# Kernel optimization log

Hardware: AMD Instinct MI355X
Metric: run time of the kernel (lower is better)

The kernel has to match this reference:

```python
import jax, jax.numpy as jnp
import numpy as np

B, S, D = 2, 2048, 1024
H, HD = 16, 64  # num_heads, head_dim; D == H*HD


def setup_inputs() -> dict:
    key = jax.random.key(0)
    k_x, k_wa, k_wp = jax.random.split(key, 3)
    x = jax.random.normal(k_x, (B, S, D), dtype=jnp.float32)
    w_attn = jax.random.normal(k_wa, (D, 3 * D), dtype=jnp.float32) * (1.0 / np.sqrt(D))
    b_attn = jnp.zeros((3 * D,), dtype=jnp.float32)
    w_proj = jax.random.normal(k_wp, (D, D), dtype=jnp.float32) * (1.0 / np.sqrt(D))
    b_proj = jnp.zeros((D,), dtype=jnp.float32)
    return {"x": x, "w_attn": w_attn, "b_attn": b_attn, "w_proj": w_proj, "b_proj": b_proj}


def reference(x, w_attn, b_attn, w_proj, b_proj):
    # c_attn: [B,S,D] -> [B,S,3D], split into q,k,v
    qkv = jnp.einsum('bsd,df->bsf', x, w_attn) + b_attn
    q, k, v = jnp.split(qkv, 3, axis=-1)
    # split heads: [B,S,D] -> [B,S,H,HD]
    q = q.reshape(B, S, H, HD)
    k = k.reshape(B, S, H, HD)
    v = v.reshape(B, S, H, HD)
    scale = 1.0 / jnp.sqrt(jnp.float32(HD))
    # scores: [B,H,S,S]
    scores = jnp.einsum('bnhd,bmhd->bhnm', q, k) * scale
    causal_mask = jnp.tril(jnp.ones((S, S), dtype=jnp.bool_))
    scores = jnp.where(causal_mask, scores, jnp.float32(-1e9))
    attn = jax.nn.softmax(scores, axis=-1)
    # dropout is identity (inference=True / p=0)
    out = jnp.einsum('bhnm,bmhd->bnhd', attn, v)
    out = out.reshape(B, S, D)
    out = jnp.einsum('bsd,de->bse', out, w_proj) + b_proj
    return out
```

## Files before the change

### kernel.cpp

```cpp
#include <hip/hip_runtime.h>

#define Bn 2
#define Sn 2048
#define Dn 1024
#define Hn 16
#define HDn 64

typedef unsigned short u16;
typedef u16 u16x4 __attribute__((ext_vector_type(4)));
typedef u16 u16x8 __attribute__((ext_vector_type(8)));
typedef __bf16 bf16x8 __attribute__((ext_vector_type(8)));
typedef float f32x4 __attribute__((ext_vector_type(4)));

__device__ __forceinline__ u16 cvt1(float f) {
  __bf16 h = (__bf16)f;
  return __builtin_bit_cast(u16, h);
}

__device__ __forceinline__ f32x4 mfma16(u16x8 a, u16x8 b, f32x4 c) {
  return __builtin_amdgcn_mfma_f32_16x16x32_bf16(
      __builtin_bit_cast(bf16x8, a), __builtin_bit_cast(bf16x8, b), c, 0, 0, 0);
}

__device__ __forceinline__ int swzb(int row, int bytecol) {
  return row * 128 + (bytecol ^ ((((row & 7) ^ ((row >> 3) & 7))) << 4));
}

__global__ __launch_bounds__(256) void k_cvt(const float* __restrict__ in,
                                             u16* __restrict__ out, int n4) {
  int i = blockIdx.x * 256 + threadIdx.x;
  if (i < n4) {
    const float4 v = reinterpret_cast<const float4*>(in)[i];
    u16x4 o = {cvt1(v.x), cvt1(v.y), cvt1(v.z), cvt1(v.w)};
    reinterpret_cast<u16x4*>(out)[i] = o;
  }
}

__global__ __launch_bounds__(256) void k_transpose(const float* __restrict__ in,
                                                   u16* __restrict__ out,
                                                   int K, int N) {
  __shared__ u16 tile[32][33];
  const int n0 = blockIdx.x * 32, k0 = blockIdx.y * 32;
  const int tx = threadIdx.x, ty = threadIdx.y;
#pragma unroll
  for (int r = 0; r < 4; ++r) {
    const int k = ty * 4 + r;
    tile[k][tx] = cvt1(in[(size_t)(k0 + k) * N + n0 + tx]);
  }
  __syncthreads();
#pragma unroll
  for (int r = 0; r < 4; ++r) {
    const int n = ty * 4 + r;
    out[(size_t)(n0 + n) * K + k0 + tx] = tile[tx][n];
  }
}

__global__ __launch_bounds__(256) void k_gemm_bt(
    const u16* __restrict__ A, const u16* __restrict__ Bt, int K,
    const float* __restrict__ bias, u16* __restrict__ oq, u16* __restrict__ ok,
    u16* __restrict__ ov, float* __restrict__ of, int mode) {
  __shared__ __align__(16) u16 a_lds[2][128 * 32];
  __shared__ __align__(16) u16 b_lds[2][128 * 32];
  const int tid = threadIdx.x;
  const int lane = tid & 63, w = tid >> 6;
  const int wr = w >> 1, wc = w & 1;
  const int lm = lane & 15, lk = lane >> 4;
  const int m0 = blockIdx.y * 128, n0 = blockIdx.x * 128;

  f32x4 acc[4][4] = {};

#define STAGE(d, ko)                                                          \
  {                                                                           \
    _Pragma("unroll") for (int p = 0; p < 2; ++p) {                           \
      const int e = p * 2048 + w * 512 + lane * 8;                            \
      const int row = e >> 5, col = e & 31;                                   \
      __builtin_amdgcn_global_load_lds(                                       \
          (const __attribute__((address_space(1))) void*)(A + (size_t)(m0 + row) * K + (ko) + col), \
          (__attribute__((address_space(3))) void*)(a_lds[d] + p * 2048 + w * 512), \
          16, 0, 0);                                                          \
      __builtin_amdgcn_global_load_lds(                                       \
          (const __attribute__((address_space(1))) void*)(Bt + (size_t)(n0 + row) * K + (ko) + col), \
          (__attribute__((address_space(3))) void*)(b_lds[d] + p * 2048 + w * 512), \
          16, 0, 0);                                                          \
    }                                                                         \
  }

  STAGE(0, 0);
  __syncthreads();
  int cur = 0;
  for (int k0 = 0; k0 < K; k0 += 32) {
    if (k0 + 32 < K) STAGE(cur ^ 1, k0 + 32);
    u16x8 av[4], bv[4];
#pragma unroll
    for (int m = 0; m < 4; ++m)
      av[m] = *reinterpret_cast<const u16x8*>(a_lds[cur] + (wr * 64 + m * 16 + lm) * 32 + lk * 8);
#pragma unroll
    for (int n = 0; n < 4; ++n)
      bv[n] = *reinterpret_cast<const u16x8*>(b_lds[cur] + (wc * 64 + n * 16 + lm) * 32 + lk * 8);
#pragma unroll
    for (int m = 0; m < 4; ++m)
#pragma unroll
      for (int n = 0; n < 4; ++n)
        acc[m][n] = mfma16(av[m], bv[n], acc[m][n]);
    __syncthreads();
    cur ^= 1;
  }
#undef STAGE

#pragma unroll
  for (int m = 0; m < 4; ++m) {
#pragma unroll
    for (int n = 0; n < 4; ++n) {
      const int col = n0 + wc * 64 + n * 16 + lm;
      const float bb = bias[col];
#pragma unroll
      for (int j = 0; j < 4; ++j) {
        const int row = m0 + wr * 64 + m * 16 + lk * 4 + j;
        float val = acc[m][n][j] + bb;
        if (mode == 0) {
          const int which = col >> 10;
          const int h = (col >> 6) & 15, hd = col & 63;
          if (which == 0) val *= 0.125f;
          const int b = row >> 11, s = row & 2047;
          const size_t idx = (((size_t)(b * Hn + h)) * Sn + s) * HDn + hd;
          u16* dst = which == 0 ? oq : (which == 1 ? ok : ov);
          dst[idx] = cvt1(val);
        } else {
          of[(size_t)row * Dn + col] = val;
        }
      }
    }
  }
}

__global__ __launch_bounds__(256) void k_attn(const u16* __restrict__ qb,
                                              const u16* __restrict__ kb,
                                              const u16* __restrict__ vb,
                                              u16* __restrict__ ob) {
  const int bx = blockIdx.x;
  const int qt = 31 - (bx >> 5);
  const int bh = bx & 31;
  const int h = bh & 15, b = bh >> 4;
  const int tid = threadIdx.x, lane = tid & 63, w = tid >> 6;
  const int lm = lane & 15, lk = lane >> 4;
  const int Q0 = qt * 64;
  const int q0 = Q0 + w * 16;
  const size_t head = (size_t)(b * Hn + h) * Sn * HDn;
  const u16* Q = qb + head;
  const u16* Kp = kb + head;
  const u16* Vp = vb + head;

  __shared__ __align__(16) u16 k_lds[64 * 64];
  __shared__ __align__(16) u16 vt_lds[64 * 64];
  __shared__ __align__(16) u16 p_lds[4][16 * 64];
  char* myp = (char*)p_lds[w];

  const int sr = tid >> 2, scb = (tid & 3) * 16;
  const u16* Ksrc = Kp + (size_t)sr * HDn + scb;
  const u16* Vsrc = Vp + (size_t)sr * HDn + scb;

  u16x8 aq[2];
#pragma unroll
  for (int c = 0; c < 2; ++c)
    aq[c] = *reinterpret_cast<const u16x8*>(Q + (size_t)(q0 + lm) * HDn + c * 32 + lk * 8);

  f32x4 o_acc[4] = {};
  float mrow = -1e30f, lrow = 0.f;
  const float C = 1.44269504f;

  const int nk = Q0 + 64;
  u16x8 kreg[2], vreg[2];
  kreg[0] = *reinterpret_cast<const u16x8*>(Ksrc);
  kreg[1] = *reinterpret_cast<const u16x8*>(Ksrc + 8);
  vreg[0] = *reinterpret_cast<const u16x8*>(Vsrc);
  vreg[1] = *reinterpret_cast<const u16x8*>(Vsrc + 8);

  for (int j0 = 0; j0 < nk; j0 += 64) {
    *reinterpret_cast<u16x8*>((char*)k_lds + swzb(sr, scb * 2)) = kreg[0];
    *reinterpret_cast<u16x8*>((char*)k_lds + swzb(sr, scb * 2 + 16)) = kreg[1];
#pragma unroll
    for (int i = 0; i < 8; ++i) {
      *reinterpret_cast<u16*>((char*)vt_lds + swzb(scb + i, sr * 2)) = vreg[0][i];
      *reinterpret_cast<u16*>((char*)vt_lds + swzb(scb + 8 + i, sr * 2)) = vreg[1][i];
    }
    __syncthreads();
    if (j0 + 64 < nk) {
      const u16* kn = Ksrc + (size_t)(j0 + 64) * HDn;
      const u16* vn = Vsrc + (size_t)(j0 + 64) * HDn;
      kreg[0] = *reinterpret_cast<const u16x8*>(kn);
      kreg[1] = *reinterpret_cast<const u16x8*>(kn + 8);
      vreg[0] = *reinterpret_cast<const u16x8*>(vn);
      vreg[1] = *reinterpret_cast<const u16x8*>(vn + 8);
    }

    f32x4 s[4];
    __builtin_amdgcn_s_setprio(1);
#pragma unroll
    for (int kc = 0; kc < 4; ++kc) {
      const u16x8 kf0 = *reinterpret_cast<const u16x8*>((char*)k_lds + swzb(kc * 16 + lm, lk * 16));
      const u16x8 kf1 = *reinterpret_cast<const u16x8*>((char*)k_lds + swzb(kc * 16 + lm, 64 + lk * 16));
      f32x4 z = {};
      z = mfma16(kf0, aq[0], z);
      s[kc] = mfma16(kf1, aq[1], z);
    }
    __builtin_amdgcn_s_setprio(0);
    if (j0 + 63 > q0) {
#pragma unroll
      for (int kc = 0; kc < 4; ++kc)
#pragma unroll
        for (int jj = 0; jj < 4; ++jj)
          if (j0 + kc * 16 + lk * 4 + jj > q0 + lm) s[kc][jj] = -1e30f;
    }

    float vmax = -1e30f;
#pragma unroll
    for (int kc = 0; kc < 4; ++kc)
#pragma unroll
      for (int jj = 0; jj < 4; ++jj) vmax = fmaxf(vmax, s[kc][jj]);
    vmax = fmaxf(vmax, __shfl_xor(vmax, 16, 64));
    vmax = fmaxf(vmax, __shfl_xor(vmax, 32, 64));
    if (!__all(vmax - mrow <= 8.0f)) {
      const float mnew = fmaxf(mrow, vmax);
      const float alpha = exp2f((mrow - mnew) * C);
      mrow = mnew;
      lrow *= alpha;
      float a4[4];
#pragma unroll
      for (int jj = 0; jj < 4; ++jj) a4[jj] = __shfl(alpha, lk * 4 + jj, 64);
#pragma unroll
      for (int t = 0; t < 4; ++t)
#pragma unroll
        for (int jj = 0; jj < 4; ++jj) o_acc[t][jj] *= a4[jj];
    }
    const float mc = mrow * C;
    float psum = 0.f;
#pragma unroll
    for (int kc = 0; kc < 4; ++kc) {
      u16x4 pk;
#pragma unroll
      for (int jj = 0; jj < 4; ++jj) {
        const float p = exp2f(s[kc][jj] * C - mc);
        psum += p;
        pk[jj] = cvt1(p);
      }
      *reinterpret_cast<u16x4*>(myp + swzb(lm, kc * 32 + lk * 8)) = pk;
    }
    psum += __shfl_xor(psum, 16, 64);
    psum += __shfl_xor(psum, 32, 64);
    lrow += psum;

    __builtin_amdgcn_s_setprio(1);
#pragma unroll
    for (int kt = 0; kt < 2; ++kt) {
      const u16x8 pa = *reinterpret_cast<const u16x8*>(myp + swzb(lm, kt * 64 + lk * 16));
#pragma unroll
      for (int t = 0; t < 4; ++t) {
        const u16x8 vf = *reinterpret_cast<const u16x8*>((char*)vt_lds + swzb(t * 16 + lm, kt * 64 + lk * 16));
        o_acc[t] = mfma16(pa, vf, o_acc[t]);
      }
    }
    __builtin_amdgcn_s_setprio(0);
    __syncthreads();
  }

  float l4[4];
#pragma unroll
  for (int jj = 0; jj < 4; ++jj) l4[jj] = __shfl(lrow, lk * 4 + jj, 64);
#pragma unroll
  for (int t = 0; t < 4; ++t) {
#pragma unroll
    for (int jj = 0; jj < 4; ++jj) {
      const int rowg = q0 + lk * 4 + jj;
      const float val = o_acc[t][jj] / l4[jj];
      ob[((size_t)(b * Sn + rowg)) * Dn + h * HDn + t * 16 + lm] = cvt1(val);
    }
  }
}

extern "C" void kernel_launch(void* const* d_in, const int* in_sizes, int n_in,
                              void* d_out, int out_size, void* d_ws, size_t ws_size,
                              hipStream_t stream) {
  const float* x = (const float*)d_in[0];
  const float* w_attn = (const float*)d_in[1];
  const float* b_attn = (const float*)d_in[2];
  const float* w_proj = (const float*)d_in[3];
  const float* b_proj = (const float*)d_in[4];
  float* out = (float*)d_out;

  u16* ws = (u16*)d_ws;
  u16* xb = ws;
  u16* wat = xb + (size_t)4096 * 1024;
  u16* wpt = wat + (size_t)3072 * 1024;
  u16* qb = wpt + (size_t)1024 * 1024;
  u16* kb = qb + (size_t)Bn * Hn * Sn * HDn;
  u16* vb = kb + (size_t)Bn * Hn * Sn * HDn;
  u16* ao = vb + (size_t)Bn * Hn * Sn * HDn;

  k_cvt<<<4096, 256, 0, stream>>>(x, xb, 1048576);
  k_transpose<<<dim3(3072 / 32, 1024 / 32), dim3(32, 8), 0, stream>>>(w_attn, wat, 1024, 3072);
  k_transpose<<<dim3(1024 / 32, 1024 / 32), dim3(32, 8), 0, stream>>>(w_proj, wpt, 1024, 1024);
  k_gemm_bt<<<dim3(3072 / 128, 4096 / 128), 256, 0, stream>>>(xb, wat, 1024, b_attn, qb, kb, vb, nullptr, 0);
  k_attn<<<Bn * Hn * (Sn / 64), 256, 0, stream>>>(qb, kb, vb, ao);
  k_gemm_bt<<<dim3(1024 / 128, 4096 / 128), 256, 0, stream>>>(ao, wpt, 1024, b_proj, nullptr, nullptr, nullptr, out, 1);
}
```

Before: 202.8 us.

## Rework GEMM to 512 threads with K=64 swizzled tiles and emit V transposed

The projection GEMM now runs 8 waves per block with a 64-wide K step, XOR-swizzled LDS staging and raised MFMA priority. This is meant to reduce LDS bank conflicts and per-iteration sync overhead. The QKV epilogue writes V in a transposed [HD][S] layout, so the attention kernel can stage V^T with vector LDS stores instead of scalar transposing stores. The trade-offs are higher LDS use per block and strided 4-element stores for V in the epilogue.

```diff
diff --git a/kernel.cpp b/kernel.cpp
--- a/kernel.cpp
+++ b/kernel.cpp
@@ -22,8 +22,11 @@
       __builtin_bit_cast(bf16x8, a), __builtin_bit_cast(bf16x8, b), c, 0, 0, 0);
 }
 
+__device__ __forceinline__ int xorv(int row) {
+  return (row & 7) ^ ((row >> 3) & 7);
+}
 __device__ __forceinline__ int swzb(int row, int bytecol) {
-  return row * 128 + (bytecol ^ ((((row & 7) ^ ((row >> 3) & 7))) << 4));
+  return row * 128 + (bytecol ^ (xorv(row) << 4));
 }
 
 __global__ __launch_bounds__(256) void k_cvt(const float* __restrict__ in,
@@ -55,79 +58,101 @@
   }
 }
 
-__global__ __launch_bounds__(256) void k_gemm_bt(
+__global__ __launch_bounds__(512) void k_gemm2(
     const u16* __restrict__ A, const u16* __restrict__ Bt, int K,
     const float* __restrict__ bias, u16* __restrict__ oq, u16* __restrict__ ok,
     u16* __restrict__ ov, float* __restrict__ of, int mode) {
-  __shared__ __align__(16) u16 a_lds[2][128 * 32];
-  __shared__ __align__(16) u16 b_lds[2][128 * 32];
+  __shared__ __align__(16) u16 a_lds[2][8192];
+  __shared__ __align__(16) u16 b_lds[2][8192];
   const int tid = threadIdx.x;
   const int lane = tid & 63, w = tid >> 6;
-  const int wr = w >> 1, wc = w & 1;
+  const int wr = w >> 2, wc = w & 3;
   const int lm = lane & 15, lk = lane >> 4;
   const int m0 = blockIdx.y * 128, n0 = blockIdx.x * 128;
-
-  f32x4 acc[4][4] = {};
-
-#define STAGE(d, ko)                                                          \
+  const int NT = K >> 6;
+
+  const int srow0 = tid >> 3;
+  const int scb = (tid & 7) * 16;
+
+  f32x4 acc[4][2] = {};
+
+#define STAGE2(d, kt)                                                         \
   {                                                                           \
     _Pragma("unroll") for (int p = 0; p < 2; ++p) {                           \
-      const int e = p * 2048 + w * 512 + lane * 8;                            \
-      const int row = e >> 5, col = e & 31;                                   \
+      const int row = p * 64 + srow0;                                         \
+      const int col = (scb ^ (xorv(row) << 4)) >> 1;                          \
       __builtin_amdgcn_global_load_lds(                                       \
-          (const __attribute__((address_space(1))) void*)(A + (size_t)(m0 + row) * K + (ko) + col), \
-          (__attribute__((address_space(3))) void*)(a_lds[d] + p * 2048 + w * 512), \
+          (const __attribute__((address_space(1))) void*)(A + (size_t)(m0 + row) * K + (kt) * 64 + col), \
+          (__attribute__((address_space(3))) void*)(a_lds[d] + p * 4096 + tid * 8), \
           16, 0, 0);                                                          \
       __builtin_amdgcn_global_load_lds(                                       \
-          (const __attribute__((address_space(1))) void*)(Bt + (size_t)(n0 + row) * K + (ko) + col), \
-          (__attribute__((address_space(3))) void*)(b_lds[d] + p * 2048 + w * 512), \
+          (const __attribute__((address_space(1))) void*)(Bt + (size_t)(n0 + row) * K + (kt) * 64 + col), \
+          (__attribute__((address_space(3))) void*)(b_lds[d] + p * 4096 + tid * 8), \
           16, 0, 0);                                                          \
     }                                                                         \
   }
 
-  STAGE(0, 0);
+  STAGE2(0, 0);
   __syncthreads();
-  int cur = 0;
-  for (int k0 = 0; k0 < K; k0 += 32) {
-    if (k0 + 32 < K) STAGE(cur ^ 1, k0 + 32);
-    u16x8 av[4], bv[4];
+
+  for (int t = 0; t < NT; ++t) {
+    const int cur = t & 1;
+    if (t + 1 < NT) STAGE2(cur ^ 1, t + 1);
+    u16x8 av[4][2], bv[2][2];
 #pragma unroll
     for (int m = 0; m < 4; ++m)
-      av[m] = *reinterpret_cast<const u16x8*>(a_lds[cur] + (wr * 64 + m * 16 + lm) * 32 + lk * 8);
-#pragma unroll
-    for (int n = 0; n < 4; ++n)
-      bv[n] = *reinterpret_cast<const u16x8*>(b_lds[cur] + (wc * 64 + n * 16 + lm) * 32 + lk * 8);
-#pragma unroll
-    for (int m = 0; m < 4; ++m)
-#pragma unroll
-      for (int n = 0; n < 4; ++n)
-        acc[m][n] = mfma16(av[m], bv[n], acc[m][n]);
+#pragma unroll
+      for (int kk = 0; kk < 2; ++kk)
+        av[m][kk] = *reinterpret_cast<const u16x8*>(
+            (char*)a_lds[cur] + swzb(wr * 64 + m * 16 + lm, kk * 64 + lk * 16));
+#pragma unroll
+    for (int n = 0; n < 2; ++n)
+#pragma unroll
+      for (int kk = 0; kk < 2; ++kk)
+        bv[n][kk] = *reinterpret_cast<const u16x8*>(
+            (char*)b_lds[cur] + swzb(wc * 32 + n * 16 + lm, kk * 64 + lk * 16));
+    __builtin_amdgcn_s_setprio(1);
+#pragma unroll
+    for (int kk = 0; kk < 2; ++kk)
+#pragma unroll
+      for (int m = 0; m < 4; ++m)
+#pragma unroll
+        for (int n = 0; n < 2; ++n)
+          acc[m][n] = mfma16(av[m][kk], bv[n][kk], acc[m][n]);
+    __builtin_amdgcn_s_setprio(0);
     __syncthreads();
-    cur ^= 1;
-  }
-#undef STAGE
+  }
+#undef STAGE2
 
 #pragma unroll
   for (int m = 0; m < 4; ++m) {
 #pragma unroll
-    for (int n = 0; n < 4; ++n) {
-      const int col = n0 + wc * 64 + n * 16 + lm;
+    for (int n = 0; n < 2; ++n) {
+      const int col = n0 + wc * 32 + n * 16 + lm;
       const float bb = bias[col];
-#pragma unroll
-      for (int j = 0; j < 4; ++j) {
-        const int row = m0 + wr * 64 + m * 16 + lk * 4 + j;
-        float val = acc[m][n][j] + bb;
-        if (mode == 0) {
-          const int which = col >> 10;
-          const int h = (col >> 6) & 15, hd = col & 63;
-          if (which == 0) val *= 0.125f;
-          const int b = row >> 11, s = row & 2047;
-          const size_t idx = (((size_t)(b * Hn + h)) * Sn + s) * HDn + hd;
-          u16* dst = which == 0 ? oq : (which == 1 ? ok : ov);
-          dst[idx] = cvt1(val);
+      const int row0 = m0 + wr * 64 + m * 16 + lk * 4;
+      if (mode == 0) {
+        const int which = col >> 10;
+        const int h = (col >> 6) & 15, hd = col & 63;
+        const int b = row0 >> 11, s0 = row0 & 2047;
+        if (which == 2) {
+          u16x4 pk;
+#pragma unroll
+          for (int j = 0; j < 4; ++j) pk[j] = cvt1(acc[m][n][j] + bb);
+          *reinterpret_cast<u16x4*>(
+              ov + ((size_t)(b * Hn + h) * HDn + hd) * Sn + s0) = pk;
         } else {
-          of[(size_t)row * Dn + col] = val;
+          u16* dst = which == 0 ? oq : ok;
+          const float sc = which == 0 ? 0.125f : 1.0f;
+#pragma unroll
+          for (int j = 0; j < 4; ++j)
+            dst[((size_t)(b * Hn + h) * Sn + s0 + j) * HDn + hd] =
+                cvt1((acc[m][n][j] + bb) * sc);
         }
+      } else {
+#pragma unroll
+        for (int j = 0; j < 4; ++j)
+          of[(size_t)(row0 + j) * Dn + col] = acc[m][n][j] + bb;
       }
     }
   }
@@ -135,7 +160,7 @@
 
 __global__ __launch_bounds__(256) void k_attn(const u16* __restrict__ qb,
                                               const u16* __restrict__ kb,
-                                              const u16* __restrict__ vb,
+                                              const u16* __restrict__ vtb,
                                               u16* __restrict__ ob) {
   const int bx = blockIdx.x;
   const int qt = 31 - (bx >> 5);
@@ -148,7 +173,7 @@
   const size_t head = (size_t)(b * Hn + h) * Sn * HDn;
   const u16* Q = qb + head;
   const u16* Kp = kb + head;
-  const u16* Vp = vb + head;
+  const u16* Vt = vtb + head;
 
   __shared__ __align__(16) u16 k_lds[64 * 64];
   __shared__ __align__(16) u16 vt_lds[64 * 64];
@@ -157,7 +182,7 @@
 
   const int sr = tid >> 2, scb = (tid & 3) * 16;
   const u16* Ksrc = Kp + (size_t)sr * HDn + scb;
-  const u16* Vsrc = Vp + (size_t)sr * HDn + scb;
+  const u16* Vsrc = Vt + (size_t)sr * Sn + scb;
 
   u16x8 aq[2];
 #pragma unroll
@@ -178,15 +203,12 @@
   for (int j0 = 0; j0 < nk; j0 += 64) {
     *reinterpret_cast<u16x8*>((char*)k_lds + swzb(sr, scb * 2)) = kreg[0];
     *reinterpret_cast<u16x8*>((char*)k_lds + swzb(sr, scb * 2 + 16)) = kreg[1];
-#pragma unroll
-    for (int i = 0; i < 8; ++i) {
-      *reinterpret_cast<u16*>((char*)vt_lds + swzb(scb + i, sr * 2)) = vreg[0][i];
-      *reinterpret_cast<u16*>((char*)vt_lds + swzb(scb + 8 + i, sr * 2)) = vreg[1][i];
-    }
+    *reinterpret_cast<u16x8*>((char*)vt_lds + swzb(sr, scb * 2)) = vreg[0];
+    *reinterpret_cast<u16x8*>((char*)vt_lds + swzb(sr, scb * 2 + 16)) = vreg[1];
     __syncthreads();
     if (j0 + 64 < nk) {
       const u16* kn = Ksrc + (size_t)(j0 + 64) * HDn;
-      const u16* vn = Vsrc + (size_t)(j0 + 64) * HDn;
+      const u16* vn = Vsrc + (j0 + 64);
       kreg[0] = *reinterpret_cast<const u16x8*>(kn);
       kreg[1] = *reinterpret_cast<const u16x8*>(kn + 8);
       vreg[0] = *reinterpret_cast<const u16x8*>(vn);
@@ -293,13 +315,13 @@
   u16* wpt = wat + (size_t)3072 * 1024;
   u16* qb = wpt + (size_t)1024 * 1024;
   u16* kb = qb + (size_t)Bn * Hn * Sn * HDn;
-  u16* vb = kb + (size_t)Bn * Hn * Sn * HDn;
-  u16* ao = vb + (size_t)Bn * Hn * Sn * HDn;
+  u16* vtb = kb + (size_t)Bn * Hn * Sn * HDn;
+  u16* ao = vtb + (size_t)Bn * Hn * Sn * HDn;
 
   k_cvt<<<4096, 256, 0, stream>>>(x, xb, 1048576);
   k_transpose<<<dim3(3072 / 32, 1024 / 32), dim3(32, 8), 0, stream>>>(w_attn, wat, 1024, 3072);
   k_transpose<<<dim3(1024 / 32, 1024 / 32), dim3(32, 8), 0, stream>>>(w_proj, wpt, 1024, 1024);
-  k_gemm_bt<<<dim3(3072 / 128, 4096 / 128), 256, 0, stream>>>(xb, wat, 1024, b_attn, qb, kb, vb, nullptr, 0);
-  k_attn<<<Bn * Hn * (Sn / 64), 256, 0, stream>>>(qb, kb, vb, ao);
-  k_gemm_bt<<<dim3(1024 / 128, 4096 / 128), 256, 0, stream>>>(ao, wpt, 1024, b_proj, nullptr, nullptr, nullptr, out, 1);
-}
+  k_gemm2<<<dim3(3072 / 128, 4096 / 128), 512, 0, stream>>>(xb, wat, 1024, b_attn, qb, kb, vtb, nullptr, 0);
+  k_attn<<<Bn * Hn * (Sn / 64), 256, 0, stream>>>(qb, kb, vtb, ao);
+  k_gemm2<<<dim3(1024 / 128, 4096 / 128), 512, 0, stream>>>(ao, wpt, 1024, b_proj, nullptr, nullptr, nullptr, out, 1);
+}
```

Measured after the change: 188.7 us. 6.9% less time.
